# Kernel tuning notes

Hardware: AMD Instinct MI355X
Metric: run time of the kernel (lower is better)

## Reference

```python
import math
import jax, jax.numpy as jnp
import numpy as np

KERNEL_SIZES = [3, 5, 7, 9, 11, 13, 15, 17]
NUM_HEADS = 2
EMBED = len(KERNEL_SIZES)  # 8
HEAD_DIM = EMBED // NUM_HEADS  # 4


def _moving_avg(x2, k):
    # x2: [B, S]; replicate-pad so output length == S (MovingAvg padding scheme)
    front = k - 1 - (k - 1) // 2
    end = (k - 1) // 2
    p = jnp.concatenate([
        jnp.repeat(x2[:, :1], front, axis=1), x2,
        jnp.repeat(x2[:, -1:], end, axis=1)
    ], axis=1)  # [B, S+k-1]
    w = jnp.full((1, 1, k), 1.0 / k, dtype=x2.dtype)
    y = jax.lax.conv_general_dilated(p[:, None, :], w, (1,), 'VALID')
    return y[:, 0, :]  # [B, S]


def setup_inputs() -> dict:
    key = jax.random.key(0)
    ks = jax.random.split(key, 6)
    B, S = 32, 2048
    D, E = HEAD_DIM, EMBED
    sd = 1.0 / math.sqrt(D)
    x = jax.random.normal(ks[0], (B, S, 1), dtype=jnp.float32)
    Wq = jax.random.normal(ks[1], (D, D), dtype=jnp.float32) * sd
    Wk = jax.random.normal(ks[2], (D, D), dtype=jnp.float32) * sd
    Wv = jax.random.normal(ks[3], (D, D), dtype=jnp.float32) * sd
    Wo = jax.random.normal(ks[4], (E, E), dtype=jnp.float32) * (1.0 / math.sqrt(E))
    bo = jax.random.normal(ks[5], (E,), dtype=jnp.float32) * 0.01
    return {"x": x, "Wq": Wq, "Wk": Wk, "Wv": Wv, "Wo": Wo, "bo": bo}


def reference(x, Wq, Wk, Wv, Wo, bo):
    B, S, _ = x.shape
    H, D, E = NUM_HEADS, HEAD_DIM, EMBED
    x2 = x[..., 0]  # [B, S]
    # multi moving-average branches -> concat on channel dim
    mm = jnp.stack([_moving_avg(x2, k) for k in KERNEL_SIZES], axis=-1)  # [B,S,E]
    t = mm.reshape(B, S, H, D)
    # nn.Linear(head_dim, head_dim, bias=False): y = x @ W^T (shared across heads)
    q = jnp.einsum('bshd,ed->bshe', t, Wq)
    k_ = jnp.einsum('bshd,ed->bshe', t, Wk)
    v = jnp.einsum('bshd,ed->bshe', t, Wv)
    scale = jnp.asarray(math.sqrt(D), dtype=x.dtype)
    energy = jnp.einsum('bqhd,bkhd->bhqk', q, k_) / scale  # [B,H,S,S]
    att = jax.nn.softmax(energy, axis=-1)  # dropout is identity in eval mode
    o = jnp.einsum('bhqk,bkhd->bqhd', att, v).reshape(B, S, E)
    o = o @ Wo.T + bo  # fc_out
    weights = jax.nn.softmax(o, axis=-1)  # [B,S,E]
    trend = jnp.sum(mm * weights, axis=-1, keepdims=True)  # [B,S,1]
    seasonal = x - trend
    return seasonal, trend
```

## Files before the change

### kernel.cpp

```cpp
#include <hip/hip_runtime.h>

#define SB 32
#define SS 2048
#define SH 2
#define SD 4
#define SE 8

#define LOG2E 1.44269504f

typedef float    f32x16 __attribute__((ext_vector_type(16)));
typedef _Float16 f16x8  __attribute__((ext_vector_type(8)));
typedef _Float16 f16x4  __attribute__((ext_vector_type(4)));

static __device__ __forceinline__ float fast_exp2(float x) {
#if __has_builtin(__builtin_amdgcn_exp2f)
    return __builtin_amdgcn_exp2f(x);
#else
    return exp2f(x);
#endif
}

static __device__ __forceinline__ int cvtpk(float a, float b) {
    auto h = __builtin_amdgcn_cvt_pkrtz(a, b);
    union { decltype(h) hh; int i; } u; u.hh = h; return u.i;
}

static __device__ __forceinline__ void swap32(int a, int b, int lane, int& r0, int& r1) {
#if __has_builtin(__builtin_amdgcn_permlane32_swap)
    auto r = __builtin_amdgcn_permlane32_swap(a, b, false, false);
    r0 = r[0]; r1 = r[1];
#else
    const int blo = __builtin_amdgcn_ds_bpermute((lane & 31) << 2, b);
    const int ahi = __builtin_amdgcn_ds_bpermute(((lane ^ 32) & 63) << 2, a);
    r0 = (lane < 32) ? a : blo;
    r1 = (lane < 32) ? ahi : b;
#endif
}

static __device__ __forceinline__ f16x8 frag2(unsigned x, unsigned y) {
    union { unsigned u[4]; f16x8 h; } c;
    c.u[0] = x; c.u[1] = y; c.u[2] = 0; c.u[3] = 0; return c.h;
}
static __device__ __forceinline__ f16x8 frag4(uint4 v) {
    union { uint4 u; f16x8 h; } c; c.u = v; return c.h;
}
static __device__ __forceinline__ f16x8 fragi(int a, int b, int c_, int d) {
    union { int u[4]; f16x8 h; } c;
    c.u[0] = a; c.u[1] = b; c.u[2] = c_; c.u[3] = d; return c.h;
}

#if __has_builtin(__builtin_amdgcn_mfma_f32_32x32x8f16)
typedef f16x4 qkfrag;
static __device__ __forceinline__ qkfrag make_qk(unsigned x, unsigned y) {
    union { unsigned u[2]; f16x4 h; } c; c.u[0] = x; c.u[1] = y; return c.h;
}
static __device__ __forceinline__ f32x16 qk_mfma(qkfrag a, qkfrag b, f32x16 c) {
    return __builtin_amdgcn_mfma_f32_32x32x8f16(a, b, c, 0, 0, 0);
}
#else
typedef f16x8 qkfrag;
static __device__ __forceinline__ qkfrag make_qk(unsigned x, unsigned y) {
    return frag2(x, y);
}
static __device__ __forceinline__ f32x16 qk_mfma(qkfrag a, qkfrag b, f32x16 c) {
    return __builtin_amdgcn_mfma_f32_32x32x16_f16(a, b, c, 0, 0, 0);
}
#endif

union u32h2 { unsigned u; _Float16 h[2]; };
static __device__ __forceinline__ unsigned packh2(float a, float b) {
    u32h2 c; c.h[0] = (_Float16)a; c.h[1] = (_Float16)b; return c.u;
}

__global__ __launch_bounds__(256) void k_ma_qkv(
    const float* __restrict__ x,
    const float* __restrict__ Wq,
    const float* __restrict__ Wk,
    const float* __restrict__ Wv,
    uint2* __restrict__ qws16,
    uint2* __restrict__ kws16,
    _Float16* __restrict__ vtg,
    float4* __restrict__ mmws)
{
    __shared__ float xs[272];

    const int tile = blockIdx.x % (SS / 256);
    const int b    = blockIdx.x / (SS / 256);
    const int s0   = tile * 256;
    const float* xrow = x + b * SS;

    for (int i = threadIdx.x; i < 272; i += 256) {
        int idx = s0 - 8 + i;
        idx = min(max(idx, 0), SS - 1);
        xs[i] = xrow[idx];
    }
    __syncthreads();

    const int t = threadIdx.x;
    const int s = s0 + t;
    const int sp = (s & ~12) | (((s >> 2) & 1) << 3) | (((s >> 3) & 1) << 2);

    float mmv[8];
    float c = xs[8 + t];
    #pragma unroll
    for (int h = 1; h <= 8; ++h) {
        c += xs[8 + t - h] + xs[8 + t + h];
        mmv[h - 1] = c * (1.0f / (float)(2 * h + 1));
    }

    mmws[(b * SS + s) * 2 + 0] = make_float4(mmv[0], mmv[1], mmv[2], mmv[3]);
    mmws[(b * SS + s) * 2 + 1] = make_float4(mmv[4], mmv[5], mmv[6], mmv[7]);

    const float qscale = 0.5f * LOG2E;
    #pragma unroll
    for (int h = 0; h < SH; ++h) {
        const float t0 = mmv[h * 4 + 0];
        const float t1 = mmv[h * 4 + 1];
        const float t2 = mmv[h * 4 + 2];
        const float t3 = mmv[h * 4 + 3];
        float q[4], k[4], v[4];
        #pragma unroll
        for (int e = 0; e < 4; ++e) {
            q[e] = (t0 * Wq[e * 4 + 0] + t1 * Wq[e * 4 + 1] +
                    t2 * Wq[e * 4 + 2] + t3 * Wq[e * 4 + 3]) * qscale;
            k[e] =  t0 * Wk[e * 4 + 0] + t1 * Wk[e * 4 + 1] +
                    t2 * Wk[e * 4 + 2] + t3 * Wk[e * 4 + 3];
            v[e] =  t0 * Wv[e * 4 + 0] + t1 * Wv[e * 4 + 1] +
                    t2 * Wv[e * 4 + 2] + t3 * Wv[e * 4 + 3];
        }
        const int bh  = b * SH + h;
        const int idx = bh * SS + s;
        qws16[idx] = make_uint2(packh2(q[0], q[1]), packh2(q[2], q[3]));
        kws16[idx] = make_uint2(packh2(k[0], k[1]), packh2(k[2], k[3]));
        #pragma unroll
        for (int e = 0; e < 4; ++e)
            vtg[(bh * 4 + e) * SS + sp] = (_Float16)v[e];
    }
}

#define LDS_K    0
#define LDS_VT   16384
#define VT_STRIDE 4112
#define LDS_Z    36944
#define LDS_SIZE 37376
#define NT       (SS / 32)

__global__ __launch_bounds__(256, 2) void k_attn(
    const uint2* __restrict__ qws16,
    const uint2* __restrict__ kws16,
    const unsigned* __restrict__ vtg,
    float4* __restrict__ ows)
{
    __shared__ __align__(16) char lds[LDS_SIZE];

    const int t    = threadIdx.x;
    const int bh   = blockIdx.x >> 3;
    const int part = blockIdx.x & 7;
    const int w    = t >> 6;
    const int ib0  = part * 8 + w;
    const int ib1  = ib0 + 4;
    const int lane = t & 63;
    const int c31  = lane & 31;

    const uint2* kg = kws16 + bh * SS;
    for (int i = t; i < SS; i += 256)
        *(uint2*)(lds + LDS_K + i * 8) = kg[i];
    const unsigned* vg = vtg + bh * 4 * (SS / 2);
    for (int i = t; i < 4 * (SS / 2); i += 256) {
        const int cc = i >> 10, col = i & 1023;
        *(unsigned*)(lds + LDS_VT + cc * VT_STRIDE + col * 4) = vg[i];
    }
    for (int i = t; i < SS / 2; i += 256)
        *(unsigned*)(lds + LDS_VT + 4 * VT_STRIDE + i * 4) = 0x3C003C00u;
    if (t < 32) *(unsigned*)(lds + LDS_Z + t * 4) = 0u;
    __syncthreads();

    uint2 qq0 = qws16[bh * SS + ib0 * 32 + c31];
    uint2 qq1 = qws16[bh * SS + ib1 * 32 + c31];
    if (lane >= 32) { qq0.x = 0u; qq0.y = 0u; qq1.x = 0u; qq1.y = 0u; }
    const qkfrag bq0 = make_qk(qq0.x, qq0.y);
    const qkfrag bq1 = make_qk(qq1.x, qq1.y);

    int kaddr = (lane < 32) ? (LDS_K + lane * 8) : LDS_Z;
    const int kstep = (lane < 32) ? 256 : 0;
    int vaddr = (c31 < 5) ? (LDS_VT + c31 * VT_STRIDE + (lane >> 5) * 16) : LDS_Z;
    const int vstep = (c31 < 5) ? 64 : 0;

    f32x16 oacc0 = {0,0,0,0,0,0,0,0,0,0,0,0,0,0,0,0};
    f32x16 oacc1 = {0,0,0,0,0,0,0,0,0,0,0,0,0,0,0,0};
    const f32x16 zc = {0,0,0,0,0,0,0,0,0,0,0,0,0,0,0,0};

    uint2 kk = *(const uint2*)(lds + kaddr); kaddr += kstep;
    f32x16 d0 = qk_mfma(make_qk(kk.x, kk.y), bq0, zc);
    f32x16 d1 = qk_mfma(make_qk(kk.x, kk.y), bq1, zc);
    kk = *(const uint2*)(lds + kaddr); kaddr += kstep;
    uint4 vv0 = *(const uint4*)(lds + vaddr);
    uint4 vv1 = *(const uint4*)(lds + vaddr + 32); vaddr += vstep;

    for (int jt = 0; jt < NT; ++jt) {
        const qkfrag ak = make_qk(kk.x, kk.y);

        {
            float p[16];
            #pragma unroll
            for (int r = 0; r < 16; ++r) p[r] = fast_exp2(d0[r]);
            d0 = qk_mfma(ak, bq0, zc);
            const f16x8 av0 = frag4(vv0);
            const f16x8 av1 = frag4(vv1);
            const int pk01 = cvtpk(p[0],  p[1]),  pk23 = cvtpk(p[2],  p[3]);
            const int pk45 = cvtpk(p[4],  p[5]),  pk67 = cvtpk(p[6],  p[7]);
            const int pk89 = cvtpk(p[8],  p[9]),  pkAB = cvtpk(p[10], p[11]);
            const int pkCD = cvtpk(p[12], p[13]), pkEF = cvtpk(p[14], p[15]);
            __builtin_amdgcn_s_setprio(1);
            oacc0 = __builtin_amdgcn_mfma_f32_32x32x16_f16(av0, fragi(pk01, pk23, pk45, pk67), oacc0, 0, 0, 0);
            oacc0 = __builtin_amdgcn_mfma_f32_32x32x16_f16(av1, fragi(pk89, pkAB, pkCD, pkEF), oacc0, 0, 0, 0);
            __builtin_amdgcn_s_setprio(0);
        }

        {
            float p[16];
            #pragma unroll
            for (int r = 0; r < 16; ++r) p[r] = fast_exp2(d1[r]);
            d1 = qk_mfma(ak, bq1, zc);
            const f16x8 av0 = frag4(vv0);
            const f16x8 av1 = frag4(vv1);
            kk  = *(const uint2*)(lds + kaddr); kaddr += kstep;
            vv0 = *(const uint4*)(lds + vaddr);
            vv1 = *(const uint4*)(lds + vaddr + 32); vaddr += vstep;
            const int pk01 = cvtpk(p[0],  p[1]),  pk23 = cvtpk(p[2],  p[3]);
            const int pk45 = cvtpk(p[4],  p[5]),  pk67 = cvtpk(p[6],  p[7]);
            const int pk89 = cvtpk(p[8],  p[9]),  pkAB = cvtpk(p[10], p[11]);
            const int pkCD = cvtpk(p[12], p[13]), pkEF = cvtpk(p[14], p[15]);
            __builtin_amdgcn_s_setprio(1);
            oacc1 = __builtin_amdgcn_mfma_f32_32x32x16_f16(av0, fragi(pk01, pk23, pk45, pk67), oacc1, 0, 0, 0);
            oacc1 = __builtin_amdgcn_mfma_f32_32x32x16_f16(av1, fragi(pk89, pkAB, pkCD, pkEF), oacc1, 0, 0, 0);
            __builtin_amdgcn_s_setprio(0);
        }
    }

    {
        union { float f; int i; } u0; u0.f = oacc0[0];
        int s0i, s1i;
        swap32(u0.i, u0.i, lane, s0i, s1i);
        union { int i; float f; } ul; ul.i = s1i;
        if (lane < 32) {
            const float inv = 1.0f / ul.f;
            ows[bh * SS + ib0 * 32 + lane] =
                make_float4(oacc0[0] * inv, oacc0[1] * inv, oacc0[2] * inv, oacc0[3] * inv);
        }
    }
    {
        union { float f; int i; } u0; u0.f = oacc1[0];
        int s0i, s1i;
        swap32(u0.i, u0.i, lane, s0i, s1i);
        union { int i; float f; } ul; ul.i = s1i;
        if (lane < 32) {
            const float inv = 1.0f / ul.f;
            ows[bh * SS + ib1 * 32 + lane] =
                make_float4(oacc1[0] * inv, oacc1[1] * inv, oacc1[2] * inv, oacc1[3] * inv);
        }
    }
}

__global__ __launch_bounds__(256) void k_epilogue(
    const float* __restrict__ x,
    const float* __restrict__ Wo,
    const float* __restrict__ bo,
    const float4* __restrict__ ows,
    const float4* __restrict__ mmws,
    float* __restrict__ out)
{
    const int pos = blockIdx.x * 256 + threadIdx.x;
    const int b = pos / SS;
    const int s = pos % SS;

    const float4 o0 = ows[(b * SH + 0) * SS + s];
    const float4 o1 = ows[(b * SH + 1) * SS + s];
    const float ov[8] = {o0.x, o0.y, o0.z, o0.w, o1.x, o1.y, o1.z, o1.w};

    float g[8];
    float m = -1e30f;
    #pragma unroll
    for (int e = 0; e < 8; ++e) {
        float acc = bo[e];
        #pragma unroll
        for (int f = 0; f < 8; ++f) acc += ov[f] * Wo[e * 8 + f];
        g[e] = acc;
        m = fmaxf(m, acc);
    }
    float l = 0.0f;
    #pragma unroll
    for (int e = 0; e < 8; ++e) { g[e] = __expf(g[e] - m); l += g[e]; }
    const float inv = 1.0f / l;

    const float4 mm0 = mmws[pos * 2 + 0];
    const float4 mm1 = mmws[pos * 2 + 1];
    const float mv[8] = {mm0.x, mm0.y, mm0.z, mm0.w, mm1.x, mm1.y, mm1.z, mm1.w};

    float trend = 0.0f;
    #pragma unroll
    for (int e = 0; e < 8; ++e) trend += g[e] * inv * mv[e];

    out[pos]           = x[pos] - trend;
    out[SB * SS + pos] = trend;
}

extern "C" void kernel_launch(void* const* d_in, const int* in_sizes, int n_in,
                              void* d_out, int out_size, void* d_ws, size_t ws_size,
                              hipStream_t stream) {
    const float* x  = (const float*)d_in[0];
    const float* Wq = (const float*)d_in[1];
    const float* Wk = (const float*)d_in[2];
    const float* Wv = (const float*)d_in[3];
    const float* Wo = (const float*)d_in[4];
    const float* bo = (const float*)d_in[5];

    uint2*     qws16 = (uint2*)d_ws;
    uint2*     kws16 = qws16 + SB * SH * SS;
    _Float16*  vtg   = (_Float16*)(kws16 + SB * SH * SS);
    float4*    mmws  = (float4*)(vtg + SB * SH * 4 * SS);
    float4*    ows   = mmws + SB * SS * 2;

    k_ma_qkv<<<SB * (SS / 256), 256, 0, stream>>>(x, Wq, Wk, Wv, qws16, kws16, vtg, mmws);
    k_attn<<<SB * SH * 8, 256, 0, stream>>>(qws16, kws16, (const unsigned*)vtg, ows);
    k_epilogue<<<(SB * SS) / 256, 256, 0, stream>>>(x, Wo, bo, ows, mmws, (float*)d_out);
}
```

Baseline: 41.82 us.

## Process four query tiles per wave in attention to reuse K/V fragments

Each wave now handles four 32-row query tiles instead of two, so every K/V fragment loaded from LDS feeds four QK and PV MFMA chains. The grid is halved to 256 blocks and launch bounds drop to one block per SIMD slot, reducing the per-block K/V LDS staging overhead and LDS read traffic per unit of work. The cost is higher register pressure from four accumulators and four score tiles, and fewer blocks, which can lower occupancy or leave CUs underused on a 256-CU part.

```diff
diff --git a/kernel.cpp b/kernel.cpp
--- a/kernel.cpp
+++ b/kernel.cpp
@@ -145,7 +145,7 @@
 #define LDS_SIZE 37376
 #define NT       (SS / 32)
 
-__global__ __launch_bounds__(256, 2) void k_attn(
+__global__ __launch_bounds__(256, 1) void k_attn(
     const uint2* __restrict__ qws16,
     const uint2* __restrict__ kws16,
     const unsigned* __restrict__ vtg,
@@ -153,14 +153,13 @@
 {
     __shared__ __align__(16) char lds[LDS_SIZE];
 
-    const int t    = threadIdx.x;
-    const int bh   = blockIdx.x >> 3;
-    const int part = blockIdx.x & 7;
-    const int w    = t >> 6;
-    const int ib0  = part * 8 + w;
-    const int ib1  = ib0 + 4;
-    const int lane = t & 63;
-    const int c31  = lane & 31;
+    const int t     = threadIdx.x;
+    const int bh    = blockIdx.x >> 2;
+    const int part  = blockIdx.x & 3;
+    const int w     = t >> 6;
+    const int ibase = (part * 4 + w) * 4;
+    const int lane  = t & 63;
+    const int c31   = lane & 31;
 
     const uint2* kg = kws16 + bh * SS;
     for (int i = t; i < SS; i += 256)
@@ -175,11 +174,18 @@
     if (t < 32) *(unsigned*)(lds + LDS_Z + t * 4) = 0u;
     __syncthreads();
 
-    uint2 qq0 = qws16[bh * SS + ib0 * 32 + c31];
-    uint2 qq1 = qws16[bh * SS + ib1 * 32 + c31];
-    if (lane >= 32) { qq0.x = 0u; qq0.y = 0u; qq1.x = 0u; qq1.y = 0u; }
+    uint2 qq0 = qws16[bh * SS + (ibase + 0) * 32 + c31];
+    uint2 qq1 = qws16[bh * SS + (ibase + 1) * 32 + c31];
+    uint2 qq2 = qws16[bh * SS + (ibase + 2) * 32 + c31];
+    uint2 qq3 = qws16[bh * SS + (ibase + 3) * 32 + c31];
+    if (lane >= 32) {
+        qq0.x = qq0.y = 0u; qq1.x = qq1.y = 0u;
+        qq2.x = qq2.y = 0u; qq3.x = qq3.y = 0u;
+    }
     const qkfrag bq0 = make_qk(qq0.x, qq0.y);
     const qkfrag bq1 = make_qk(qq1.x, qq1.y);
+    const qkfrag bq2 = make_qk(qq2.x, qq2.y);
+    const qkfrag bq3 = make_qk(qq3.x, qq3.y);
 
     int kaddr = (lane < 32) ? (LDS_K + lane * 8) : LDS_Z;
     const int kstep = (lane < 32) ? 256 : 0;
@@ -188,25 +194,29 @@
 
     f32x16 oacc0 = {0,0,0,0,0,0,0,0,0,0,0,0,0,0,0,0};
     f32x16 oacc1 = {0,0,0,0,0,0,0,0,0,0,0,0,0,0,0,0};
+    f32x16 oacc2 = {0,0,0,0,0,0,0,0,0,0,0,0,0,0,0,0};
+    f32x16 oacc3 = {0,0,0,0,0,0,0,0,0,0,0,0,0,0,0,0};
     const f32x16 zc = {0,0,0,0,0,0,0,0,0,0,0,0,0,0,0,0};
 
     uint2 kk = *(const uint2*)(lds + kaddr); kaddr += kstep;
     f32x16 d0 = qk_mfma(make_qk(kk.x, kk.y), bq0, zc);
     f32x16 d1 = qk_mfma(make_qk(kk.x, kk.y), bq1, zc);
+    f32x16 d2 = qk_mfma(make_qk(kk.x, kk.y), bq2, zc);
+    f32x16 d3 = qk_mfma(make_qk(kk.x, kk.y), bq3, zc);
     kk = *(const uint2*)(lds + kaddr); kaddr += kstep;
     uint4 vv0 = *(const uint4*)(lds + vaddr);
     uint4 vv1 = *(const uint4*)(lds + vaddr + 32); vaddr += vstep;
 
     for (int jt = 0; jt < NT; ++jt) {
-        const qkfrag ak = make_qk(kk.x, kk.y);
+        const qkfrag ak  = make_qk(kk.x, kk.y);
+        const f16x8  av0 = frag4(vv0);
+        const f16x8  av1 = frag4(vv1);
 
         {
             float p[16];
             #pragma unroll
             for (int r = 0; r < 16; ++r) p[r] = fast_exp2(d0[r]);
             d0 = qk_mfma(ak, bq0, zc);
-            const f16x8 av0 = frag4(vv0);
-            const f16x8 av1 = frag4(vv1);
             const int pk01 = cvtpk(p[0],  p[1]),  pk23 = cvtpk(p[2],  p[3]);
             const int pk45 = cvtpk(p[4],  p[5]),  pk67 = cvtpk(p[6],  p[7]);
             const int pk89 = cvtpk(p[8],  p[9]),  pkAB = cvtpk(p[10], p[11]);
@@ -216,14 +226,39 @@
             oacc0 = __builtin_amdgcn_mfma_f32_32x32x16_f16(av1, fragi(pk89, pkAB, pkCD, pkEF), oacc0, 0, 0, 0);
             __builtin_amdgcn_s_setprio(0);
         }
-
         {
             float p[16];
             #pragma unroll
             for (int r = 0; r < 16; ++r) p[r] = fast_exp2(d1[r]);
             d1 = qk_mfma(ak, bq1, zc);
-            const f16x8 av0 = frag4(vv0);
-            const f16x8 av1 = frag4(vv1);
+            const int pk01 = cvtpk(p[0],  p[1]),  pk23 = cvtpk(p[2],  p[3]);
+            const int pk45 = cvtpk(p[4],  p[5]),  pk67 = cvtpk(p[6],  p[7]);
+            const int pk89 = cvtpk(p[8],  p[9]),  pkAB = cvtpk(p[10], p[11]);
+            const int pkCD = cvtpk(p[12], p[13]), pkEF = cvtpk(p[14], p[15]);
+            __builtin_amdgcn_s_setprio(1);
+            oacc1 = __builtin_amdgcn_mfma_f32_32x32x16_f16(av0, fragi(pk01, pk23, pk45, pk67), oacc1, 0, 0, 0);
+            oacc1 = __builtin_amdgcn_mfma_f32_32x32x16_f16(av1, fragi(pk89, pkAB, pkCD, pkEF), oacc1, 0, 0, 0);
+            __builtin_amdgcn_s_setprio(0);
+        }
+        {
+            float p[16];
+            #pragma unroll
+            for (int r = 0; r < 16; ++r) p[r] = fast_exp2(d2[r]);
+            d2 = qk_mfma(ak, bq2, zc);
+            const int pk01 = cvtpk(p[0],  p[1]),  pk23 = cvtpk(p[2],  p[3]);
+            const int pk45 = cvtpk(p[4],  p[5]),  pk67 = cvtpk(p[6],  p[7]);
+            const int pk89 = cvtpk(p[8],  p[9]),  pkAB = cvtpk(p[10], p[11]);
+            const int pkCD = cvtpk(p[12], p[13]), pkEF = cvtpk(p[14], p[15]);
+            __builtin_amdgcn_s_setprio(1);
+            oacc2 = __builtin_amdgcn_mfma_f32_32x32x16_f16(av0, fragi(pk01, pk23, pk45, pk67), oacc2, 0, 0, 0);
+            oacc2 = __builtin_amdgcn_mfma_f32_32x32x16_f16(av1, fragi(pk89, pkAB, pkCD, pkEF), oacc2, 0, 0, 0);
+            __builtin_amdgcn_s_setprio(0);
+        }
+        {
+            float p[16];
+            #pragma unroll
+            for (int r = 0; r < 16; ++r) p[r] = fast_exp2(d3[r]);
+            d3 = qk_mfma(ak, bq3, zc);
             kk  = *(const uint2*)(lds + kaddr); kaddr += kstep;
             vv0 = *(const uint4*)(lds + vaddr);
             vv1 = *(const uint4*)(lds + vaddr + 32); vaddr += vstep;
@@ -232,34 +267,30 @@
             const int pk89 = cvtpk(p[8],  p[9]),  pkAB = cvtpk(p[10], p[11]);
             const int pkCD = cvtpk(p[12], p[13]), pkEF = cvtpk(p[14], p[15]);
             __builtin_amdgcn_s_setprio(1);
-            oacc1 = __builtin_amdgcn_mfma_f32_32x32x16_f16(av0, fragi(pk01, pk23, pk45, pk67), oacc1, 0, 0, 0);
-            oacc1 = __builtin_amdgcn_mfma_f32_32x32x16_f16(av1, fragi(pk89, pkAB, pkCD, pkEF), oacc1, 0, 0, 0);
+            oacc3 = __builtin_amdgcn_mfma_f32_32x32x16_f16(av0, fragi(pk01, pk23, pk45, pk67), oacc3, 0, 0, 0);
+            oacc3 = __builtin_amdgcn_mfma_f32_32x32x16_f16(av1, fragi(pk89, pkAB, pkCD, pkEF), oacc3, 0, 0, 0);
             __builtin_amdgcn_s_setprio(0);
         }
     }
 
-    {
-        union { float f; int i; } u0; u0.f = oacc0[0];
-        int s0i, s1i;
-        swap32(u0.i, u0.i, lane, s0i, s1i);
-        union { int i; float f; } ul; ul.i = s1i;
-        if (lane < 32) {
-            const float inv = 1.0f / ul.f;
-            ows[bh * SS + ib0 * 32 + lane] =
-                make_float4(oacc0[0] * inv, oacc0[1] * inv, oacc0[2] * inv, oacc0[3] * inv);
-        }
-    }
-    {
-        union { float f; int i; } u0; u0.f = oacc1[0];
-        int s0i, s1i;
-        swap32(u0.i, u0.i, lane, s0i, s1i);
-        union { int i; float f; } ul; ul.i = s1i;
-        if (lane < 32) {
-            const float inv = 1.0f / ul.f;
-            ows[bh * SS + ib1 * 32 + lane] =
-                make_float4(oacc1[0] * inv, oacc1[1] * inv, oacc1[2] * inv, oacc1[3] * inv);
-        }
-    }
+    #define WRITE_OUT(OACC, IB)                                                \
+    {                                                                          \
+        union { float f; int i; } u0; u0.f = (OACC)[0];                        \
+        int s0i, s1i;                                                          \
+        swap32(u0.i, u0.i, lane, s0i, s1i);                                    \
+        union { int i; float f; } ul; ul.i = s1i;                              \
+        if (lane < 32) {                                                       \
+            const float inv = 1.0f / ul.f;                                     \
+            ows[bh * SS + (IB) * 32 + lane] =                                  \
+                make_float4((OACC)[0] * inv, (OACC)[1] * inv,                  \
+                            (OACC)[2] * inv, (OACC)[3] * inv);                 \
+        }                                                                      \
+    }
+    WRITE_OUT(oacc0, ibase + 0)
+    WRITE_OUT(oacc1, ibase + 1)
+    WRITE_OUT(oacc2, ibase + 2)
+    WRITE_OUT(oacc3, ibase + 3)
+    #undef WRITE_OUT
 }
 
 __global__ __launch_bounds__(256) void k_epilogue(
@@ -322,6 +353,6 @@
     float4*    ows   = mmws + SB * SS * 2;
 
     k_ma_qkv<<<SB * (SS / 256), 256, 0, stream>>>(x, Wq, Wk, Wv, qws16, kws16, vtg, mmws);
-    k_attn<<<SB * SH * 8, 256, 0, stream>>>(qws16, kws16, (const unsigned*)vtg, ows);
+    k_attn<<<SB * SH * 4, 256, 0, stream>>>(qws16, kws16, (const unsigned*)vtg, ows);
     k_epilogue<<<(SB * SS) / 256, 256, 0, stream>>>(x, Wo, bo, ows, mmws, (float*)d_out);
 }
```

After: 48.89 us. +16.9%, slower.
